# Kernel optimization log

Hardware: AMD Instinct MI355X
Metric: run time of the kernel (lower is better)

The kernel has to match this reference:

```python
import jax, jax.numpy as jnp
import numpy as np
from jax import lax

N = 4096        # batch
NP = 16         # num_puzzle (4x4 grid)
P = 8           # size_puzzle (patch side)
GRID = 4        # sqrt(num_puzzle)
HW = GRID * P   # 32


def _shuffle_patches(x, noise):
    # x: [N, C, H, W]; noise: [N, NP]
    ids_shuffle = jnp.argsort(noise, axis=1)            # [N, NP]
    ids_restore = jnp.argsort(ids_shuffle, axis=1)      # [N, NP]
    n_, c, h, w = x.shape
    # -> [N, GRID(row), P, GRID(col), P] per channel, patches in row-major order
    patches = x.reshape(n_, c, GRID, P, GRID, P)
    patches = patches.transpose(0, 2, 4, 1, 3, 5).reshape(n_, NP, c, P, P)
    shuffled = jnp.take_along_axis(patches, ids_shuffle[:, :, None, None, None], axis=1)
    # reassemble: new patch j goes to grid slot j (row-major)
    img = shuffled.reshape(n_, GRID, GRID, c, P, P).transpose(0, 3, 1, 4, 2, 5)
    img = img.reshape(n_, c, h, w)
    return img, ids_restore


def _conv(x, w, b):
    y = lax.conv_general_dilated(x, w, window_strides=(1, 1), padding='SAME',
                                 dimension_numbers=('NCHW', 'OIHW', 'NCHW'))
    return y + b[None, :, None, None]


def _maxpool2(x):
    return lax.reduce_window(x, -jnp.inf, lax.max, (1, 1, 2, 2), (1, 1, 2, 2), 'VALID')


def setup_inputs() -> dict:
    key = jax.random.key(0)
    ks = jax.random.split(key, 16)
    s = 0.05
    inp = {
        'x': jax.random.normal(ks[0], (N, 3, HW, HW), dtype=jnp.float32),
        'noise': jax.random.uniform(ks[1], (N, NP), dtype=jnp.float32),
        'conv1_w': jax.random.normal(ks[2], (32, 3, 3, 3), dtype=jnp.float32) * s,
        'conv1_b': jnp.zeros((32,), dtype=jnp.float32),
        'conv2_w': jax.random.normal(ks[3], (64, 32, 3, 3), dtype=jnp.float32) * s,
        'conv2_b': jnp.zeros((64,), dtype=jnp.float32),
        'conv3_w': jax.random.normal(ks[4], (128, 64, 3, 3), dtype=jnp.float32) * s,
        'conv3_b': jnp.zeros((128,), dtype=jnp.float32),
        'fc1_w': jax.random.normal(ks[5], (128 * 4 * 4, 1024), dtype=jnp.float32) * s,
        'fc1_b': jnp.zeros((1024,), dtype=jnp.float32),
        'fc2_w': jax.random.normal(ks[6], (1024, 1024), dtype=jnp.float32) * s,
        'fc2_b': jnp.zeros((1024,), dtype=jnp.float32),
        'fc3_w': jax.random.normal(ks[7], (1024, 1024), dtype=jnp.float32) * s,
        'fc3_b': jnp.zeros((1024,), dtype=jnp.float32),
        'fc4_w': jax.random.normal(ks[8], (1024, 1024), dtype=jnp.float32) * s,
        'fc4_b': jnp.zeros((1024,), dtype=jnp.float32),
        'fc5_w': jax.random.normal(ks[9], (1024, NP * NP), dtype=jnp.float32) * s,
        'fc5_b': jnp.zeros((NP * NP,), dtype=jnp.float32),
    }
    return inp


def reference(x, noise, conv1_w, conv1_b, conv2_w, conv2_b, conv3_w, conv3_b,
              fc1_w, fc1_b, fc2_w, fc2_b, fc3_w, fc3_b, fc4_w, fc4_b, fc5_w, fc5_b):
    x, target = _shuffle_patches(x, noise)
    x = _maxpool2(jax.nn.relu(_conv(x, conv1_w, conv1_b)))   # [N,32,16,16]
    x = _maxpool2(jax.nn.relu(_conv(x, conv2_w, conv2_b)))   # [N,64,8,8]
    x = _maxpool2(jax.nn.relu(_conv(x, conv3_w, conv3_b)))   # [N,128,4,4]
    x = x.reshape(-1, 128 * 4 * 4)
    x = jax.nn.relu(x @ fc1_w + fc1_b)
    x = jax.nn.relu(x @ fc2_w + fc2_b)
    x = jax.nn.relu(x @ fc3_w + fc3_b)
    x = jax.nn.relu(x @ fc4_w + fc4_b)
    x = x @ fc5_w + fc5_b
    x = x.reshape(-1, NP, NP)
    return x, target
```

## Files before the change

kernel.cpp:

```cpp
#include <hip/hip_runtime.h>

#define BATCH 4096
#define NPATCH 16

typedef __attribute__((ext_vector_type(8)))  short  short8;
typedef __attribute__((ext_vector_type(4)))  float  f32x4;
typedef unsigned short ushort_t;

__device__ __forceinline__ ushort_t f2bf(float f) {
    union { float f; unsigned u; } x; x.f = f;
    unsigned r = x.u + 0x7FFFu + ((x.u >> 16) & 1u);
    return (ushort_t)(r >> 16);
}

__device__ __forceinline__ void gload_lds16(const void* g, void* l) {
    __builtin_amdgcn_global_load_lds((const __attribute__((address_space(1))) void*)g,
                                     (__attribute__((address_space(3))) void*)l, 16, 0, 0);
}

__global__ void rank_kernel(const float* __restrict__ noise,
                            int* __restrict__ ids_shuffle,
                            float* __restrict__ target_out) {
    int n = blockIdx.x * 256 + threadIdx.x;
    if (n >= BATCH) return;
    float v[NPATCH];
#pragma unroll
    for (int i = 0; i < NPATCH; i++) v[i] = noise[n * NPATCH + i];
#pragma unroll
    for (int j = 0; j < NPATCH; j++) {
        int r = 0;
#pragma unroll
        for (int i = 0; i < NPATCH; i++)
            if (v[i] < v[j] || (v[i] == v[j] && i < j)) r++;
        ids_shuffle[n * NPATCH + r] = j;
        target_out[n * NPATCH + j] = (float)r;
    }
}

__global__ void prep_convw(const float* __restrict__ W, ushort_t* __restrict__ WT,
                           int OC, int IC, int ICP, int KWP) {
    int KP = 3 * KWP * ICP;
    int i = blockIdx.x * 256 + threadIdx.x;
    if (i >= OC * KP) return;
    int oc = i / KP, k = i % KP;
    int kh = k / (KWP * ICP);
    int kw = (k / ICP) % KWP;
    int ic = k % ICP;
    ushort_t v = 0;
    if (kw < 3 && ic < IC)
        v = f2bf(W[((oc * IC + ic) * 3 + kh) * 3 + kw]);
    WT[i] = v;
}

__global__ void transpose_w(const float* __restrict__ W, ushort_t* __restrict__ WT,
                            int K, int N) {
    __shared__ ushort_t t[32][33];
    int kb = blockIdx.x * 32, nb = blockIdx.y * 32;
    int tx = threadIdx.x & 31, ty = threadIdx.x >> 5;
#pragma unroll
    for (int i = 0; i < 32; i += 8)
        t[ty + i][tx] = f2bf(W[(size_t)(kb + ty + i) * N + nb + tx]);
    __syncthreads();
#pragma unroll
    for (int i = 0; i < 32; i += 8)
        WT[(size_t)(nb + ty + i) * K + kb + tx] = t[tx][ty + i];
}

__global__ void transpose_w_fc1(const float* __restrict__ W, ushort_t* __restrict__ WT) {
    __shared__ ushort_t t[32][33];
    int kb = blockIdx.x * 32, nb = blockIdx.y * 32;
    int hw = kb >> 7, c0 = kb & 127;
    int tx = threadIdx.x & 31, ty = threadIdx.x >> 5;
#pragma unroll
    for (int i = 0; i < 32; i += 8)
        t[ty + i][tx] = f2bf(W[(size_t)((c0 + ty + i) * 16 + hw) * 1024 + nb + tx]);
    __syncthreads();
#pragma unroll
    for (int i = 0; i < 32; i += 8)
        WT[(size_t)(nb + ty + i) * 2048 + kb + tx] = t[tx][ty + i];
}

__global__ __launch_bounds__(256, 4)
void shuffle_conv1(const float* __restrict__ x, const int* __restrict__ ids,
                   const ushort_t* __restrict__ WT, const float* __restrict__ bias,
                   ushort_t* __restrict__ Y) {
    __shared__ ushort_t Xs[4 * 32 * 39 * 4];
    const int tid = threadIdx.x;
    const int wid = tid >> 6, lane = tid & 63;
    const int l15 = lane & 15, l4 = lane >> 4;
    const int b = blockIdx.x;
    const int xcd = b & 7, s = b >> 3;
    const int ph = s & 15;
    const int n0 = (((s >> 4) << 3) + xcd) << 5;
    const int wn = wid & 1, wp = wid >> 1;

#pragma unroll
    for (int it = 0; it < 2; ++it) {
        int task = it * 256 + tid;
        int rr = task >> 7;
        int nl = (task >> 2) & 31;
        int q  = task & 3;
        int ih = 2 * ph - 1 + rr;
        int n  = n0 + nl;
        ushort_t* row = &Xs[(rr * 32 + nl) * 39 * 4];
        {
            const unsigned z2[2] = {0, 0};
            if (q == 0) {
                *(uint2*)&row[0] = *(const uint2*)z2;
            } else {
                int base = 31 + q * 2;
                *(uint2*)&row[base * 4]       = *(const uint2*)z2;
                *(uint2*)&row[(base + 1) * 4] = *(const uint2*)z2;
            }
        }
        f32x4 v0a = {0.f,0.f,0.f,0.f}, v0b = v0a, v1a = v0a, v1b = v0a, v2a = v0a, v2b = v0a;
        if ((unsigned)ih < 32u) {
            int j  = ((ih >> 3) << 2) | q;
            int p  = ids[(n << 4) + j];
            int sh = ((p >> 2) << 3) | (ih & 7);
            int sw = (p & 3) << 3;
            const float* src = x + (size_t)n * 3072 + (sh << 5) + sw;
            v0a = *(const f32x4*)(src);        v0b = *(const f32x4*)(src + 4);
            v1a = *(const f32x4*)(src + 1024); v1b = *(const f32x4*)(src + 1028);
            v2a = *(const f32x4*)(src + 2048); v2b = *(const f32x4*)(src + 2052);
        }
        ushort_t* dst = &row[(q * 8 + 1) * 4];
#pragma unroll
        for (int e = 0; e < 8; ++e) {
            float f0 = (e < 4) ? v0a[e & 3] : v0b[e & 3];
            float f1 = (e < 4) ? v1a[e & 3] : v1b[e & 3];
            float f2 = (e < 4) ? v2a[e & 3] : v2b[e & 3];
            ushort_t u[4] = {f2bf(f0), f2bf(f1), f2bf(f2), 0};
            *(uint2*)&dst[e * 4] = *(const uint2*)u;
        }
    }

    short8 af[3][2];
#pragma unroll
    for (int kh = 0; kh < 3; ++kh)
#pragma unroll
        for (int i = 0; i < 2; ++i)
            af[kh][i] = *(const short8*)(WT + (i * 16 + l15) * 96 + kh * 32 + l4 * 8);

    __syncthreads();

    const int nlb = wn * 16 + l15;
    const int n = n0 + nlb;

#pragma unroll
    for (int pwl = 0; pwl < 8; ++pwl) {
        int pw = wp * 8 + pwl;
        f32x4 accp[2][4];
#pragma unroll
        for (int i = 0; i < 2; ++i)
#pragma unroll
            for (int p = 0; p < 4; ++p)
#pragma unroll
                for (int r = 0; r < 4; ++r) accp[i][p][r] = 0.f;

#pragma unroll
        for (int pc = 0; pc < 2; ++pc)
#pragma unroll
            for (int rr = 0; rr < 4; ++rr) {
                int w2 = 2 * pw + pc + 2 * l4;
                const ushort_t* pB = &Xs[((rr * 32 + nlb) * 39 + w2) * 4];
                short8 bf;
                *(uint2*)&bf       = *(const uint2*)pB;
                *(((uint2*)&bf)+1) = *(const uint2*)(pB + 4);
#pragma unroll
                for (int pr = 0; pr < 2; ++pr) {
                    int kh = rr - pr;
                    if (kh < 0 || kh > 2) continue;
#pragma unroll
                    for (int i = 0; i < 2; ++i)
                        accp[i][pr * 2 + pc] = __builtin_amdgcn_mfma_f32_16x16x32_bf16(
                            af[kh][i], bf, accp[i][pr * 2 + pc], 0, 0, 0);
                }
            }

#pragma unroll
        for (int i = 0; i < 2; ++i) {
            int ocb = i * 16 + l4 * 4;
            ushort_t u[4];
#pragma unroll
            for (int r = 0; r < 4; ++r) {
                float mx = fmaxf(fmaxf(accp[i][0][r], accp[i][1][r]),
                                 fmaxf(accp[i][2][r], accp[i][3][r]));
                u[r] = f2bf(fmaxf(mx + bias[ocb + r], 0.f));
            }
            *(uint2*)(Y + ((size_t)(ph * 16 + pw) * 4096 + n) * 32 + ocb) = *(const uint2*)u;
        }
    }
}

__global__ __launch_bounds__(256, 2)
void conv2_gemm(const ushort_t* __restrict__ X, const ushort_t* __restrict__ WT,
                const float* __restrict__ bias, ushort_t* __restrict__ Y) {
    __shared__ ushort_t Bs[2][4 * 64 * 32];
    const int tid = threadIdx.x;
    const int wid = tid >> 6, lane = tid & 63;
    const int l15 = lane & 15, l4 = lane >> 4;
    const int orig = blockIdx.x;
    const int lin = (orig & 7) * 512 + (orig >> 3);
    const int pos = lin & 63;
    const int n0 = (lin >> 6) * 64;
    const int ph = pos >> 3, pw = pos & 7;

    short8 af[9];
#pragma unroll
    for (int t = 0; t < 9; ++t)
        af[t] = *(const short8*)(WT + (size_t)(wid * 16 + l15) * 288 + (t * 4 + l4) * 8);

    f32x4 acc[4][4];
#pragma unroll
    for (int p = 0; p < 4; ++p)
#pragma unroll
        for (int j = 0; j < 4; ++j)
#pragma unroll
            for (int r = 0; r < 4; ++r) acc[p][j][r] = 0.f;

    {
        int ih = 2 * ph - 1;
        if (ih >= 0) {
#pragma unroll
            for (int dw = 0; dw < 4; ++dw) {
                int iw = 2 * pw - 1 + dw;
                if ((unsigned)iw >= 16u) continue;
                int m = tid >> 2, ss = tid & 3;
                int cc = ss ^ ((m >> 1) & 3);
                gload_lds16(X + ((size_t)(ih * 16 + iw) * 4096 + n0 + m) * 32 + cc * 8,
                            &Bs[0][dw * 2048 + wid * 512]);
            }
        }
    }
    __syncthreads();

#pragma unroll
    for (int r = 0; r < 4; ++r) {
        const int cur = r & 1;
        if (r < 3) {
            int ihn = 2 * ph + r;
            if (ihn < 16) {
#pragma unroll
                for (int dw = 0; dw < 4; ++dw) {
                    int iw = 2 * pw - 1 + dw;
                    if ((unsigned)iw >= 16u) continue;
                    int m = tid >> 2, ss = tid & 3;
                    int cc = ss ^ ((m >> 1) & 3);
                    gload_lds16(X + ((size_t)(ihn * 16 + iw) * 4096 + n0 + m) * 32 + cc * 8,
                                &Bs[cur ^ 1][dw * 2048 + wid * 512]);
                }
            }
        }
        int ih = 2 * ph - 1 + r;
        if ((unsigned)ih < 16u) {
#pragma unroll
            for (int dw = 0; dw < 4; ++dw) {
                int iw = 2 * pw - 1 + dw;
                if ((unsigned)iw >= 16u) continue;
                short8 bf[4];
#pragma unroll
                for (int j = 0; j < 4; ++j) {
                    int m2 = j * 16 + l15;
                    bf[j] = *(const short8*)(
                        &Bs[cur][(dw * 64 + m2) * 32 + ((l4 ^ ((m2 >> 1) & 3)) * 8)]);
                }
#pragma unroll
                for (int pr = 0; pr < 2; ++pr) {
                    int kh = r - pr;
                    if (kh < 0 || kh > 2) continue;
#pragma unroll
                    for (int pc = 0; pc < 2; ++pc) {
                        int kw = dw - pc;
                        if (kw < 0 || kw > 2) continue;
                        int tap = kh * 3 + kw;
#pragma unroll
                        for (int j = 0; j < 4; ++j)
                            acc[pr * 2 + pc][j] =
                                __builtin_amdgcn_mfma_f32_16x16x32_bf16(
                                    af[tap], bf[j], acc[pr * 2 + pc][j], 0, 0, 0);
                    }
                }
            }
        }
        __syncthreads();
    }

    {
        int oc_l = wid * 16 + l4 * 4;
#pragma unroll
        for (int j = 0; j < 4; ++j) {
            int n = n0 + j * 16 + l15;
            ushort_t u[4];
#pragma unroll
            for (int r = 0; r < 4; ++r) {
                float mx = fmaxf(fmaxf(acc[0][j][r], acc[1][j][r]),
                                 fmaxf(acc[2][j][r], acc[3][j][r]));
                u[r] = f2bf(fmaxf(mx + bias[oc_l + r], 0.f));
            }
            *(uint2*)(Y + ((size_t)pos * 4096 + n) * 64 + oc_l) = *(const uint2*)u;
        }
    }
}

template <int IC, int H, int OC, bool FC_EPI, int MINB>
__global__ __launch_bounds__(256, MINB)
void conv_gemm(const ushort_t* __restrict__ X, const ushort_t* __restrict__ WT,
               const float* __restrict__ bias, ushort_t* __restrict__ Y) {
    constexpr int PW = H / 2;
    constexpr int K  = 9 * IC;
    constexpr int CH = IC / 8;
    constexpr int CM = CH - 1;
    constexpr int KK = IC / 32;
    constexpr int WM = (OC == 128) ? 2 : 1;
    constexpr int WN = 4 / WM;
    constexpr int WTM = OC / WM / 16;
    constexpr int WTN = 128 / WN / 16;
    constexpr int APASS = OC * CH / 256;
    constexpr int BPASS = 128 * CH / 256;
    constexpr int NPOS = PW * PW;

    __shared__ ushort_t As[OC * IC];
    __shared__ ushort_t Bs[128 * IC];
    const int tid = threadIdx.x;
    const int wid = tid >> 6, lane = tid & 63;
    const int wm = wid / WN, wn = wid % WN;
    const int l15 = lane & 15, l4 = lane >> 4;
    const int orig = blockIdx.x;
    const int nwg = NPOS * 32;
    const int lin = (orig & 7) * (nwg / 8) + (orig >> 3);
    const int ph = (lin % NPOS) / PW, pw = (lin % NPOS) % PW;
    const int n0 = (lin / NPOS) * 128;

    f32x4 acc[WTM][WTN], mx[WTM][WTN];

    for (int p = 0; p < 4; ++p) {
#pragma unroll
        for (int i = 0; i < WTM; ++i)
#pragma unroll
            for (int j = 0; j < WTN; ++j)
#pragma unroll
                for (int r = 0; r < 4; ++r) acc[i][j][r] = 0.f;
        const int pr = p >> 1, pc = p & 1;
        for (int t = 0; t < 9; ++t) {
            const int kh = t / 3, kw = t % 3;
            const int ih = 2 * ph + pr - 1 + kh;
            const int iw = 2 * pw + pc - 1 + kw;
            if ((unsigned)ih >= (unsigned)H || (unsigned)iw >= (unsigned)H) continue;
            __syncthreads();
            const ushort_t* bsrc = X + (size_t)(ih * H + iw) * 4096 * IC + (size_t)n0 * IC;
#pragma unroll
            for (int pass = 0; pass < APASS; ++pass) {
                int idx = pass * 256 + tid;
                int m = idx / CH, ss = idx % CH;
                int cc = ss ^ (m & CM);
                gload_lds16(WT + (size_t)m * K + t * IC + cc * 8,
                            &As[(pass * 256 + wid * 64) * 8]);
            }
#pragma unroll
            for (int pass = 0; pass < BPASS; ++pass) {
                int idx = pass * 256 + tid;
                int m = idx / CH, ss = idx % CH;
                int cc = ss ^ (m & CM);
                gload_lds16(bsrc + (size_t)m * IC + cc * 8,
                            &Bs[(pass * 256 + wid * 64) * 8]);
            }
            __syncthreads();
#pragma unroll
            for (int kk = 0; kk < KK; ++kk) {
                short8 af[WTM], bf[WTN];
                int c = kk * 4 + l4;
#pragma unroll
                for (int i = 0; i < WTM; ++i) {
                    int m = wm * (WTM * 16) + i * 16 + l15;
                    af[i] = *(const short8*)(As + m * IC + ((c ^ (m & CM)) * 8));
                }
#pragma unroll
                for (int j = 0; j < WTN; ++j) {
                    int m = wn * (WTN * 16) + j * 16 + l15;
                    bf[j] = *(const short8*)(Bs + m * IC + ((c ^ (m & CM)) * 8));
                }
#pragma unroll
                for (int i = 0; i < WTM; ++i)
#pragma unroll
                    for (int j = 0; j < WTN; ++j)
                        acc[i][j] = __builtin_amdgcn_mfma_f32_16x16x32_bf16(
                            af[i], bf[j], acc[i][j], 0, 0, 0);
            }
        }
#pragma unroll
        for (int i = 0; i < WTM; ++i)
#pragma unroll
            for (int j = 0; j < WTN; ++j)
#pragma unroll
                for (int r = 0; r < 4; ++r)
                    mx[i][j][r] = (p == 0) ? acc[i][j][r]
                                           : fmaxf(mx[i][j][r], acc[i][j][r]);
    }

#pragma unroll
    for (int i = 0; i < WTM; ++i) {
        int oc_l = wm * (WTM * 16) + i * 16 + l4 * 4;
#pragma unroll
        for (int j = 0; j < WTN; ++j) {
            int n = n0 + wn * (WTN * 16) + j * 16 + l15;
            ushort_t u[4];
#pragma unroll
            for (int r = 0; r < 4; ++r)
                u[r] = f2bf(fmaxf(mx[i][j][r] + bias[oc_l + r], 0.f));
            if (FC_EPI)
                *(uint2*)(Y + (size_t)n * 2048 + (ph * 4 + pw) * 128 + oc_l) = *(const uint2*)u;
            else
                *(uint2*)(Y + ((size_t)(ph * PW + pw) * 4096 + n) * OC + oc_l) = *(const uint2*)u;
        }
    }
}

template <bool RELU, bool F32OUT>
__global__ __launch_bounds__(256, 2)
void fc_mfma(const ushort_t* __restrict__ A, const ushort_t* __restrict__ BT,
             const float* __restrict__ bias, void* __restrict__ Cout,
             int M, int N, int K) {
    __shared__ ushort_t As[2][128 * 64];
    __shared__ ushort_t Bs[2][64 * 64];
    const int tid = threadIdx.x;
    const int wid = tid >> 6, lane = tid & 63;
    const int wr = wid >> 1, wc = wid & 1;
    const int tm = blockIdx.y * 128, tn = blockIdx.x * 64;
    const int l15 = lane & 15, l4 = lane >> 4;

    f32x4 acc[4][2];
#pragma unroll
    for (int i = 0; i < 4; ++i)
#pragma unroll
        for (int j = 0; j < 2; ++j)
#pragma unroll
            for (int r = 0; r < 4; ++r) acc[i][j][r] = 0.f;

    const int NT = K >> 6;
#pragma unroll
    for (int pass = 0; pass < 4; ++pass) {
        int m = pass * 32 + (tid >> 3);
        int cc = (tid & 7) ^ (m & 7);
        gload_lds16(A + (size_t)(tm + m) * K + cc * 8,
                    &As[0][(pass * 256 + wid * 64) * 8]);
    }
#pragma unroll
    for (int pass = 0; pass < 2; ++pass) {
        int m = pass * 32 + (tid >> 3);
        int cc = (tid & 7) ^ (m & 7);
        gload_lds16(BT + (size_t)(tn + m) * K + cc * 8,
                    &Bs[0][(pass * 256 + wid * 64) * 8]);
    }
    __syncthreads();

    for (int t = 0; t < NT; ++t) {
        const int cur = t & 1, nxt = cur ^ 1;
        if (t + 1 < NT) {
            const int k1 = (t + 1) << 6;
#pragma unroll
            for (int pass = 0; pass < 4; ++pass) {
                int m = pass * 32 + (tid >> 3);
                int cc = (tid & 7) ^ (m & 7);
                gload_lds16(A + (size_t)(tm + m) * K + k1 + cc * 8,
                            &As[nxt][(pass * 256 + wid * 64) * 8]);
            }
#pragma unroll
            for (int pass = 0; pass < 2; ++pass) {
                int m = pass * 32 + (tid >> 3);
                int cc = (tid & 7) ^ (m & 7);
                gload_lds16(BT + (size_t)(tn + m) * K + k1 + cc * 8,
                            &Bs[nxt][(pass * 256 + wid * 64) * 8]);
            }
        }
#pragma unroll
        for (int kk = 0; kk < 2; ++kk) {
            short8 af[4], bfr[2];
            int c = kk * 4 + l4;
#pragma unroll
            for (int i = 0; i < 4; ++i) {
                int m = wr * 64 + i * 16 + l15;
                af[i] = *(const short8*)(&As[cur][m * 64 + (c ^ (m & 7)) * 8]);
            }
#pragma unroll
            for (int j = 0; j < 2; ++j) {
                int nn = wc * 32 + j * 16 + l15;
                bfr[j] = *(const short8*)(&Bs[cur][nn * 64 + (c ^ (nn & 7)) * 8]);
            }
#pragma unroll
            for (int i = 0; i < 4; ++i)
#pragma unroll
                for (int j = 0; j < 2; ++j)
                    acc[i][j] = __builtin_amdgcn_mfma_f32_16x16x32_bf16(
                        af[i], bfr[j], acc[i][j], 0, 0, 0);
        }
        __syncthreads();
    }

#pragma unroll
    for (int i = 0; i < 4; ++i) {
        int row = tm + wr * 64 + i * 16 + l4 * 4;
#pragma unroll
        for (int j = 0; j < 2; ++j) {
            int col = tn + wc * 32 + j * 16 + l15;
            float bv = bias[col];
#pragma unroll
            for (int r = 0; r < 4; ++r) {
                float v = acc[i][j][r] + bv;
                if (RELU) v = fmaxf(v, 0.f);
                if (F32OUT)
                    ((float*)Cout)[(size_t)(row + r) * N + col] = v;
                else
                    ((ushort_t*)Cout)[(size_t)(row + r) * N + col] = f2bf(v);
            }
        }
    }
}

extern "C" void kernel_launch(void* const* d_in, const int* in_sizes, int n_in,
                              void* d_out, int out_size, void* d_ws, size_t ws_size,
                              hipStream_t stream) {
    const float* x     = (const float*)d_in[0];
    const float* noise = (const float*)d_in[1];
    const float* c1w = (const float*)d_in[2];  const float* c1b = (const float*)d_in[3];
    const float* c2w = (const float*)d_in[4];  const float* c2b = (const float*)d_in[5];
    const float* c3w = (const float*)d_in[6];  const float* c3b = (const float*)d_in[7];
    const float* f1w = (const float*)d_in[8];  const float* f1b = (const float*)d_in[9];
    const float* f2w = (const float*)d_in[10]; const float* f2b = (const float*)d_in[11];
    const float* f3w = (const float*)d_in[12]; const float* f3b = (const float*)d_in[13];
    const float* f4w = (const float*)d_in[14]; const float* f4b = (const float*)d_in[15];
    const float* f5w = (const float*)d_in[16]; const float* f5b = (const float*)d_in[17];
    float* out = (float*)d_out;

    char* ws = (char*)d_ws;
    const size_t MB = 1ull << 20;
    int*      ids  = (int*)ws;
    ushort_t* wc1  = (ushort_t*)(ws + 1 * MB);
    ushort_t* wc2  = (ushort_t*)(ws + 1 * MB + 64 * 1024);
    ushort_t* wc3  = (ushort_t*)(ws + 1 * MB + 128 * 1024);
    ushort_t* wf1  = (ushort_t*)(ws + 2 * MB);
    ushort_t* wf2  = (ushort_t*)(ws + 6 * MB);
    ushort_t* wf3  = (ushort_t*)(ws + 8 * MB);
    ushort_t* wf4  = (ushort_t*)(ws + 10 * MB);
    ushort_t* wf5  = (ushort_t*)(ws + 12 * MB);
    ushort_t* act1 = (ushort_t*)(ws + 89 * MB);
    ushort_t* act2 = (ushort_t*)(ws + 153 * MB);
    ushort_t* act3 = (ushort_t*)(ws + 185 * MB);
    ushort_t* fcb1 = (ushort_t*)(ws + 201 * MB);
    ushort_t* fcb2 = (ushort_t*)(ws + 209 * MB);

    prep_convw<<<(32 * 96 + 255) / 256, 256, 0, stream>>>(c1w, wc1, 32, 3, 4, 8);
    prep_convw<<<(64 * 288 + 255) / 256, 256, 0, stream>>>(c2w, wc2, 64, 32, 32, 3);
    prep_convw<<<(128 * 576 + 255) / 256, 256, 0, stream>>>(c3w, wc3, 128, 64, 64, 3);
    transpose_w_fc1<<<dim3(64, 32), 256, 0, stream>>>(f1w, wf1);
    transpose_w<<<dim3(32, 32), 256, 0, stream>>>(f2w, wf2, 1024, 1024);
    transpose_w<<<dim3(32, 32), 256, 0, stream>>>(f3w, wf3, 1024, 1024);
    transpose_w<<<dim3(32, 32), 256, 0, stream>>>(f4w, wf4, 1024, 1024);
    transpose_w<<<dim3(32, 8),  256, 0, stream>>>(f5w, wf5, 1024, 256);

    rank_kernel<<<BATCH / 256, 256, 0, stream>>>(noise, ids, out + (size_t)BATCH * 256);
    shuffle_conv1<<<dim3(2048), 256, 0, stream>>>(x, ids, wc1, c1b, act1);

    conv2_gemm<<<dim3(4096), 256, 0, stream>>>(act1, wc2, c2b, act2);
    conv_gemm<64, 8, 128, true, 2><<<dim3(512), 256, 0, stream>>>(act2, wc3, c3b, act3);

    fc_mfma<true,  false><<<dim3(16, 32), 256, 0, stream>>>(act3, wf1, f1b, fcb1, BATCH, 1024, 2048);
    fc_mfma<true,  false><<<dim3(16, 32), 256, 0, stream>>>(fcb1, wf2, f2b, fcb2, BATCH, 1024, 1024);
    fc_mfma<true,  false><<<dim3(16, 32), 256, 0, stream>>>(fcb2, wf3, f3b, fcb1, BATCH, 1024, 1024);
    fc_mfma<true,  false><<<dim3(16, 32), 256, 0, stream>>>(fcb1, wf4, f4b, fcb2, BATCH, 1024, 1024);
    fc_mfma<false, true ><<<dim3(4, 32),  256, 0, stream>>>(fcb2, wf5, f5b, out, BATCH, 256, 1024);
}
```

Measured before the change: 252.2 us.

## Merge weight-prep launches into one kernel and split conv3 output channels

The eight separate weight conversion and transpose launches are folded into a single prep_all kernel that picks its sub-task from the block index, removing per-launch overhead. conv3 now splits its 128 output channels into two 64-channel groups, doubling the grid to 1024 workgroups and raising the min-blocks occupancy hint from 2 to 4. This is meant to fill the GPU better for conv3 and cut launch gaps, at the cost of loading each activation tile twice, once per channel group.

```diff
diff --git a/kernel.cpp b/kernel.cpp
--- a/kernel.cpp
+++ b/kernel.cpp
@@ -37,47 +37,59 @@
     }
 }
 
-__global__ void prep_convw(const float* __restrict__ W, ushort_t* __restrict__ WT,
-                           int OC, int IC, int ICP, int KWP) {
+__device__ __forceinline__ void prep_elem(const float* W, ushort_t* WT, int idx,
+                                          int IC, int ICP, int KWP) {
     int KP = 3 * KWP * ICP;
-    int i = blockIdx.x * 256 + threadIdx.x;
-    if (i >= OC * KP) return;
-    int oc = i / KP, k = i % KP;
+    int oc = idx / KP, k = idx % KP;
     int kh = k / (KWP * ICP);
     int kw = (k / ICP) % KWP;
     int ic = k % ICP;
     ushort_t v = 0;
     if (kw < 3 && ic < IC)
         v = f2bf(W[((oc * IC + ic) * 3 + kh) * 3 + kw]);
-    WT[i] = v;
-}
-
-__global__ void transpose_w(const float* __restrict__ W, ushort_t* __restrict__ WT,
-                            int K, int N) {
+    WT[idx] = v;
+}
+
+__global__ void prep_all(const float* __restrict__ c1w, const float* __restrict__ c2w,
+                         const float* __restrict__ c3w, const float* __restrict__ f1w,
+                         const float* __restrict__ f2w, const float* __restrict__ f3w,
+                         const float* __restrict__ f4w, const float* __restrict__ f5w,
+                         ushort_t* wc1, ushort_t* wc2, ushort_t* wc3,
+                         ushort_t* wf1, ushort_t* wf2, ushort_t* wf3,
+                         ushort_t* wf4, ushort_t* wf5) {
     __shared__ ushort_t t[32][33];
-    int kb = blockIdx.x * 32, nb = blockIdx.y * 32;
-    int tx = threadIdx.x & 31, ty = threadIdx.x >> 5;
-#pragma unroll
-    for (int i = 0; i < 32; i += 8)
-        t[ty + i][tx] = f2bf(W[(size_t)(kb + ty + i) * N + nb + tx]);
+    int b = blockIdx.x;
+    int tid = threadIdx.x;
+    if (b < 372) {
+        int idx = b * 256 + tid;
+        if (idx < 3072)        prep_elem(c1w, wc1, idx, 3, 4, 8);
+        else if (idx < 21504)  prep_elem(c2w, wc2, idx - 3072, 32, 32, 3);
+        else if (idx < 95232)  prep_elem(c3w, wc3, idx - 21504, 64, 64, 3);
+        return;
+    }
+    b -= 372;
+    const float* W; ushort_t* WT; int K, N, ntk; bool fc1 = false; int tile;
+    if (b < 2048)      { fc1 = true; tile = b;        W = f1w; WT = wf1; K = 2048; N = 1024; ntk = 64; }
+    else if (b < 3072) { tile = b - 2048;             W = f2w; WT = wf2; K = 1024; N = 1024; ntk = 32; }
+    else if (b < 4096) { tile = b - 3072;             W = f3w; WT = wf3; K = 1024; N = 1024; ntk = 32; }
+    else if (b < 5120) { tile = b - 4096;             W = f4w; WT = wf4; K = 1024; N = 1024; ntk = 32; }
+    else               { tile = b - 5120;             W = f5w; WT = wf5; K = 1024; N = 256;  ntk = 32; }
+    int kb = (tile % ntk) * 32, nb = (tile / ntk) * 32;
+    int tx = tid & 31, ty = tid >> 5;
+    if (!fc1) {
+#pragma unroll
+        for (int i = 0; i < 32; i += 8)
+            t[ty + i][tx] = f2bf(W[(size_t)(kb + ty + i) * N + nb + tx]);
+    } else {
+        int hw = kb >> 7, c0 = kb & 127;
+#pragma unroll
+        for (int i = 0; i < 32; i += 8)
+            t[ty + i][tx] = f2bf(W[(size_t)((c0 + ty + i) * 16 + hw) * 1024 + nb + tx]);
+    }
     __syncthreads();
 #pragma unroll
     for (int i = 0; i < 32; i += 8)
         WT[(size_t)(nb + ty + i) * K + kb + tx] = t[tx][ty + i];
-}
-
-__global__ void transpose_w_fc1(const float* __restrict__ W, ushort_t* __restrict__ WT) {
-    __shared__ ushort_t t[32][33];
-    int kb = blockIdx.x * 32, nb = blockIdx.y * 32;
-    int hw = kb >> 7, c0 = kb & 127;
-    int tx = threadIdx.x & 31, ty = threadIdx.x >> 5;
-#pragma unroll
-    for (int i = 0; i < 32; i += 8)
-        t[ty + i][tx] = f2bf(W[(size_t)((c0 + ty + i) * 16 + hw) * 1024 + nb + tx]);
-    __syncthreads();
-#pragma unroll
-    for (int i = 0; i < 32; i += 8)
-        WT[(size_t)(nb + ty + i) * 2048 + kb + tx] = t[tx][ty + i];
 }
 
 __global__ __launch_bounds__(256, 4)
@@ -303,34 +315,38 @@
     }
 }
 
-template <int IC, int H, int OC, bool FC_EPI, int MINB>
+template <int IC, int H, int OCB, int OCT, bool FC_EPI, int MINB>
 __global__ __launch_bounds__(256, MINB)
-void conv_gemm(const ushort_t* __restrict__ X, const ushort_t* __restrict__ WT,
-               const float* __restrict__ bias, ushort_t* __restrict__ Y) {
+void conv3_gemm(const ushort_t* __restrict__ X, const ushort_t* __restrict__ WT,
+                const float* __restrict__ bias, ushort_t* __restrict__ Y) {
     constexpr int PW = H / 2;
     constexpr int K  = 9 * IC;
     constexpr int CH = IC / 8;
     constexpr int CM = CH - 1;
     constexpr int KK = IC / 32;
-    constexpr int WM = (OC == 128) ? 2 : 1;
+    constexpr int NSPLIT = OCT / OCB;
+    constexpr int NPOS = PW * PW;
+    constexpr int NWG = NPOS * 32 * NSPLIT;
+    constexpr int WM = (OCB == 128) ? 2 : 1;
     constexpr int WN = 4 / WM;
-    constexpr int WTM = OC / WM / 16;
+    constexpr int WTM = OCB / WM / 16;
     constexpr int WTN = 128 / WN / 16;
-    constexpr int APASS = OC * CH / 256;
+    constexpr int APASS = OCB * CH / 256;
     constexpr int BPASS = 128 * CH / 256;
-    constexpr int NPOS = PW * PW;
-
-    __shared__ ushort_t As[OC * IC];
+
+    __shared__ ushort_t As[OCB * IC];
     __shared__ ushort_t Bs[128 * IC];
     const int tid = threadIdx.x;
     const int wid = tid >> 6, lane = tid & 63;
     const int wm = wid / WN, wn = wid % WN;
     const int l15 = lane & 15, l4 = lane >> 4;
     const int orig = blockIdx.x;
-    const int nwg = NPOS * 32;
-    const int lin = (orig & 7) * (nwg / 8) + (orig >> 3);
-    const int ph = (lin % NPOS) / PW, pw = (lin % NPOS) % PW;
-    const int n0 = (lin / NPOS) * 128;
+    const int lin = (orig & 7) * (NWG / 8) + (orig >> 3);
+    const int ocg = lin % NSPLIT;
+    const int rem = lin / NSPLIT;
+    const int ph = (rem % NPOS) / PW, pw = (rem % NPOS) % PW;
+    const int n0 = (rem / NPOS) * 128;
+    const int ocbase = ocg * OCB;
 
     f32x4 acc[WTM][WTN], mx[WTM][WTN];
 
@@ -354,7 +370,7 @@
                 int idx = pass * 256 + tid;
                 int m = idx / CH, ss = idx % CH;
                 int cc = ss ^ (m & CM);
-                gload_lds16(WT + (size_t)m * K + t * IC + cc * 8,
+                gload_lds16(WT + (size_t)(ocbase + m) * K + t * IC + cc * 8,
                             &As[(pass * 256 + wid * 64) * 8]);
             }
 #pragma unroll
@@ -400,7 +416,7 @@
 
 #pragma unroll
     for (int i = 0; i < WTM; ++i) {
-        int oc_l = wm * (WTM * 16) + i * 16 + l4 * 4;
+        int oc_l = ocbase + wm * (WTM * 16) + i * 16 + l4 * 4;
 #pragma unroll
         for (int j = 0; j < WTN; ++j) {
             int n = n0 + wn * (WTN * 16) + j * 16 + l15;
@@ -411,7 +427,7 @@
             if (FC_EPI)
                 *(uint2*)(Y + (size_t)n * 2048 + (ph * 4 + pw) * 128 + oc_l) = *(const uint2*)u;
             else
-                *(uint2*)(Y + ((size_t)(ph * PW + pw) * 4096 + n) * OC + oc_l) = *(const uint2*)u;
+                *(uint2*)(Y + ((size_t)(ph * PW + pw) * 4096 + n) * OCT + oc_l) = *(const uint2*)u;
         }
     }
 }
@@ -549,20 +565,14 @@
     ushort_t* fcb1 = (ushort_t*)(ws + 201 * MB);
     ushort_t* fcb2 = (ushort_t*)(ws + 209 * MB);
 
-    prep_convw<<<(32 * 96 + 255) / 256, 256, 0, stream>>>(c1w, wc1, 32, 3, 4, 8);
-    prep_convw<<<(64 * 288 + 255) / 256, 256, 0, stream>>>(c2w, wc2, 64, 32, 32, 3);
-    prep_convw<<<(128 * 576 + 255) / 256, 256, 0, stream>>>(c3w, wc3, 128, 64, 64, 3);
-    transpose_w_fc1<<<dim3(64, 32), 256, 0, stream>>>(f1w, wf1);
-    transpose_w<<<dim3(32, 32), 256, 0, stream>>>(f2w, wf2, 1024, 1024);
-    transpose_w<<<dim3(32, 32), 256, 0, stream>>>(f3w, wf3, 1024, 1024);
-    transpose_w<<<dim3(32, 32), 256, 0, stream>>>(f4w, wf4, 1024, 1024);
-    transpose_w<<<dim3(32, 8),  256, 0, stream>>>(f5w, wf5, 1024, 256);
+    prep_all<<<dim3(5748), 256, 0, stream>>>(c1w, c2w, c3w, f1w, f2w, f3w, f4w, f5w,
+                                             wc1, wc2, wc3, wf1, wf2, wf3, wf4, wf5);
 
     rank_kernel<<<BATCH / 256, 256, 0, stream>>>(noise, ids, out + (size_t)BATCH * 256);
     shuffle_conv1<<<dim3(2048), 256, 0, stream>>>(x, ids, wc1, c1b, act1);
 
     conv2_gemm<<<dim3(4096), 256, 0, stream>>>(act1, wc2, c2b, act2);
-    conv_gemm<64, 8, 128, true, 2><<<dim3(512), 256, 0, stream>>>(act2, wc3, c3b, act3);
+    conv3_gemm<64, 8, 64, 128, true, 4><<<dim3(1024), 256, 0, stream>>>(act2, wc3, c3b, act3);
 
     fc_mfma<true,  false><<<dim3(16, 32), 256, 0, stream>>>(act3, wf1, f1b, fcb1, BATCH, 1024, 2048);
     fc_mfma<true,  false><<<dim3(16, 32), 256, 0, stream>>>(fcb1, wf2, f2b, fcb2, BATCH, 1024, 1024);
```

Result: slower. 266.6 us (+5.7%).
